# Performance work log

Measured on AMD Instinct MI355X. Metric: run time of the kernel, lower is better.

Reference implementation:

```python
import jax, jax.numpy as jnp
import numpy as np

B, T, INP, OUT, H = 64, 512, 256, 256, 512


def _uniform(key, shape, scale):
    return jax.random.uniform(key, shape, jnp.float32, -scale, scale)


def lstm_proj(x, w_ih, w_hh, b, w_hr):
    """Single-layer LSTM with projection (torch nn.LSTM proj_size semantics).
    x: [B,T,D], w_ih: [4H,D], w_hh: [4H,P], b: [4H] (b_ih+b_hh), w_hr: [P,H].
    Returns hidden sequence [B,T,P]. Gate order: i, f, g, o."""
    # Precompute input contribution for all timesteps: [T,B,4H]
    xg = jnp.einsum('btd,gd->tbg', x, w_ih) + b
    Bsz = x.shape[0]
    P, Hh = w_hr.shape
    h0 = jnp.zeros((Bsz, P), x.dtype)
    c0 = jnp.zeros((Bsz, Hh), x.dtype)

    def step(carry, xg_t):
        h, c = carry
        gates = xg_t + h @ w_hh.T          # [B,4H]
        i, f, g, o = jnp.split(gates, 4, axis=-1)
        c = jax.nn.sigmoid(f) * c + jax.nn.sigmoid(i) * jnp.tanh(g)
        h = (jax.nn.sigmoid(o) * jnp.tanh(c)) @ w_hr.T  # projected hidden [B,P]
        return (h, c), h

    _, hs = jax.lax.scan(step, (h0, c0), xg)
    return hs.transpose(1, 0, 2)  # [B,T,P]


def setup_inputs() -> dict:
    key = jax.random.key(0)
    ks = jax.random.split(key, 10)
    s = 1.0 / np.sqrt(H)
    inp = jax.random.normal(ks[0], (B, T, INP), jnp.float32)
    out = jax.random.normal(ks[1], (B, T, OUT), jnp.float32)
    # lstm: input INP -> hidden H, proj OUT
    w_ih1 = _uniform(ks[2], (4 * H, INP), s)
    w_hh1 = _uniform(ks[3], (4 * H, OUT), s)
    b1 = _uniform(ks[4], (4 * H,), s) * 2.0  # b_ih + b_hh combined
    w_hr1 = _uniform(ks[5], (OUT, H), s)
    # lstm_reverse: input OUT -> hidden H, proj INP
    w_ih2 = _uniform(ks[6], (4 * H, OUT), s)
    w_hh2 = _uniform(ks[7], (4 * H, INP), s)
    b2 = _uniform(ks[8], (4 * H,), s) * 2.0
    w_hr2 = _uniform(ks[9], (INP, H), s)
    return {"inp": inp, "out": out,
            "w_ih1": w_ih1, "w_hh1": w_hh1, "b1": b1, "w_hr1": w_hr1,
            "w_ih2": w_ih2, "w_hh2": w_hh2, "b2": b2, "w_hr2": w_hr2}


def reference(inp, out, w_ih1, w_hh1, b1, w_hr1, w_ih2, w_hh2, b2, w_hr2):
    out2 = lstm_proj(inp, w_ih1, w_hh1, b1, w_hr1)   # [B,T,OUT]
    inp2 = lstm_proj(out, w_ih2, w_hh2, b2, w_hr2)   # [B,T,INP]
    return (inp2, out2)
```

## Files before the change

kernel.cpp:

```cpp
#include <hip/hip_runtime.h>

constexpr int kB = 64, kT = 512, kD = 256, kH = 512, kG = 2048;
constexpr int kNB = 256, kNT = 256;

typedef __attribute__((ext_vector_type(8))) short bf16x8;
typedef __attribute__((ext_vector_type(4))) float f32x4;
typedef unsigned long long ull;
union U4 { unsigned u[4]; ull q[2]; bf16x8 v; };

__device__ __forceinline__ ushort f2bf(float x) {
    union { float f; unsigned u; } v; v.f = x;
    unsigned r = v.u + 0x7FFFu + ((v.u >> 16) & 1u);
    return (ushort)(r >> 16);
}
__device__ __forceinline__ unsigned pk2(float a, float b) {
    return (unsigned)f2bf(a) | ((unsigned)f2bf(b) << 16);
}
__device__ __forceinline__ float sigm(float x) { return 1.f / (1.f + __expf(-x)); }

#define AT_LOAD(p)     __hip_atomic_load((p), __ATOMIC_RELAXED, __HIP_MEMORY_SCOPE_AGENT)
#define AT_LOAD64(p)   __hip_atomic_load((p), __ATOMIC_RELAXED, __HIP_MEMORY_SCOPE_AGENT)
#define AT_STORE(p,v)  __hip_atomic_store((p), (v), __ATOMIC_RELAXED, __HIP_MEMORY_SCOPE_AGENT)
#define AT_ADD(p,v)    __hip_atomic_fetch_add((p), (v), __ATOMIC_RELAXED, __HIP_MEMORY_SCOPE_AGENT)
#define VMCNT0() asm volatile("s_waitcnt vmcnt(0)" ::: "memory")

__device__ __forceinline__ unsigned ld_dw(const unsigned* p, bool fast) {
    unsigned r;
    if (fast) asm volatile("global_load_dword %0, %1, off sc0\n\ts_waitcnt vmcnt(0)"
                           : "=&v"(r) : "v"(p) : "memory");
    else r = AT_LOAD(p);
    return r;
}
__device__ __forceinline__ void ld8q(const ull* p, ull* q, bool fast) {
    if (fast) {
        asm volatile(
            "global_load_dwordx2 %0, %8, off sc0\n\t"
            "global_load_dwordx2 %1, %8, off offset:8 sc0\n\t"
            "global_load_dwordx2 %2, %8, off offset:16 sc0\n\t"
            "global_load_dwordx2 %3, %8, off offset:24 sc0\n\t"
            "global_load_dwordx2 %4, %8, off offset:32 sc0\n\t"
            "global_load_dwordx2 %5, %8, off offset:40 sc0\n\t"
            "global_load_dwordx2 %6, %8, off offset:48 sc0\n\t"
            "global_load_dwordx2 %7, %8, off offset:56 sc0\n\t"
            "s_waitcnt vmcnt(0)"
            : "=&v"(q[0]), "=&v"(q[1]), "=&v"(q[2]), "=&v"(q[3]),
              "=&v"(q[4]), "=&v"(q[5]), "=&v"(q[6]), "=&v"(q[7])
            : "v"(p) : "memory");
    } else {
        #pragma unroll
        for (int i = 0; i < 8; i++) q[i] = AT_LOAD64(p + i);
    }
}
__device__ __forceinline__ void st_u16(ushort* p, ushort v, bool fast) {
    if (fast) *p = v;
    else __hip_atomic_store(p, v, __ATOMIC_RELAXED, __HIP_MEMORY_SCOPE_AGENT);
}
__device__ __forceinline__ void st_dw(unsigned* p, unsigned v, bool fast) {
    if (fast) *p = v;
    else AT_STORE(p, v);
}

__global__ void bar_init_kernel(unsigned* ws) {
    AT_STORE(ws + threadIdx.x, 0u);
}

__global__ void __launch_bounds__(kNT, 1) lstm2_kernel(
    const float* __restrict__ x1, const float* __restrict__ x2,
    const float* __restrict__ wih1, const float* __restrict__ whh1,
    const float* __restrict__ b1,   const float* __restrict__ whr1,
    const float* __restrict__ wih2, const float* __restrict__ whh2,
    const float* __restrict__ b2,   const float* __restrict__ whr2,
    float* __restrict__ out, unsigned* __restrict__ ws)
{
    const int bid = blockIdx.x, tid = threadIdx.x;
    const int team = bid & 7, rank = bid >> 3;
    const int l = team >> 2, bteam = team & 3, blkh = rank;
    const int h0 = blkh * 16, grow0 = bteam * 16;

    const float* x   = l ? x2 : x1;
    const float* wih = l ? wih2 : wih1;
    const float* whh = l ? whh2 : whh1;
    const float* bb  = l ? b2 : b1;
    const float* whr = l ? whr2 : whr1;
    float* outp = out + (l ? (size_t)0 : (size_t)kB * kT * kD);

    unsigned* TG  = ws + 256;
    unsigned* XC  = ws + 768;
    unsigned* SDB = ws + 1024;
    unsigned* WC  = ws + 66560;

    __shared__ unsigned sst[16 * 268];
    __shared__ float lgs[4][16][17];

    __builtin_amdgcn_fence(__ATOMIC_SEQ_CST, "agent");
    VMCNT0();

    unsigned xcc;
    asm volatile("s_getreg_b32 %0, hwreg(HW_REG_XCC_ID)" : "=s"(xcc));
    xcc &= 15u;
    if (tid == 0) AT_STORE(XC + bid, xcc);

    {
        const int wlin = bteam * 32 + rank;
        const int j  = wlin * 16 + (tid >> 4);
        const int k0 = (tid & 15) * 32;
        const float* whh_r = whh + (size_t)j * kD;
        float acc[32];
        #pragma unroll
        for (int i = 0; i < 32; i++) acc[i] = 0.f;
        for (int p = 0; p < kD; p++) {
            float w = whh_r[p];
            const float4* wr = (const float4*)(whr + (size_t)p * kH + k0);
            #pragma unroll
            for (int q = 0; q < 8; q++) {
                float4 v = wr[q];
                acc[q*4+0] = fmaf(w, v.x, acc[q*4+0]);
                acc[q*4+1] = fmaf(w, v.y, acc[q*4+1]);
                acc[q*4+2] = fmaf(w, v.z, acc[q*4+2]);
                acc[q*4+3] = fmaf(w, v.w, acc[q*4+3]);
            }
        }
        unsigned* dst = WC + (size_t)l * kG * 256 + (size_t)j * 256 + k0 / 2;
        #pragma unroll
        for (int i = 0; i < 16; i++) AT_STORE(dst + i, pk2(acc[2*i], acc[2*i+1]));
    }
    VMCNT0();
    __syncthreads();
    if (tid == 0) {
        unsigned a = AT_ADD(ws + 0, 1u);
        if (a == (unsigned)(kNB - 1)) AT_STORE(ws + 64, 1u);
        while (AT_LOAD(ws + 64) == 0u) __builtin_amdgcn_s_sleep(2);
    }
    __syncthreads();

    const int lane = tid & 63;
    unsigned x0 = AT_LOAD(XC + team);
    unsigned xr = (lane < 32) ? AT_LOAD(XC + team + 8 * lane) : x0;
    const bool fast = __all((int)(xr == x0));

    if (rank == 0 && tid < 64) st_dw(TG + team * 64 + tid, 0u, fast);
    if (tid < 128) {
        st_dw(SDB + (size_t)(team * 2 + 0) * 4096 + rank * 128 + tid, 0u, fast);
        st_dw(SDB + (size_t)(team * 2 + 1) * 4096 + rank * 128 + tid, 0u, fast);
    }

    const int wv = tid >> 6;
    const int n = lane & 15, kq = lane >> 4;
    const int gcol = wv * kH + h0 + n;
    const float bias = bb[gcol];
    const int mrow = grow0 + n;
    const int crow = tid >> 4, ccol = tid & 15;

    bf16x8 bxh[8];
    #pragma unroll
    for (int ks = 0; ks < 8; ks++) {
        const float4* p = (const float4*)(wih + (size_t)gcol * kD + ks * 32 + kq * 8);
        float4 a0 = p[0], a1 = p[1];
        U4 h;
        h.u[0] = pk2(a0.x, a0.y); h.u[1] = pk2(a0.z, a0.w);
        h.u[2] = pk2(a1.x, a1.y); h.u[3] = pk2(a1.z, a1.w);
        bxh[ks] = h.v;
    }
    bf16x8 bsh[16];
    {
        const ull* wcp = (const ull*)(WC + (size_t)l * kG * 256 + (size_t)gcol * 256);
        #pragma unroll
        for (int ks = 0; ks < 16; ks++) {
            U4 u;
            u.q[0] = AT_LOAD64(wcp + ks * 8 + kq * 2 + 0);
            u.q[1] = AT_LOAD64(wcp + ks * 8 + kq * 2 + 1);
            bsh[ks] = u.v;
        }
    }
    const bool isProj = (blkh < 16);
    bf16x8 bp[16];
    if (isProj) {
        const int pcol = blkh * 16 + n;
        #pragma unroll
        for (int ks = 0; ks < 16; ks++) {
            const float4* p = (const float4*)(whr + (size_t)pcol * kH + ks * 32 + kq * 8);
            float4 a0 = p[0], a1 = p[1];
            U4 h;
            h.u[0] = pk2(a0.x, a0.y); h.u[1] = pk2(a0.z, a0.w);
            h.u[2] = pk2(a1.x, a1.y); h.u[3] = pk2(a1.z, a1.w);
            bp[ks] = h.v;
        }
    }
    bf16x8 ax[8];
    #pragma unroll
    for (int ks = 0; ks < 8; ks++) {
        const float4* xp = (const float4*)(x + (size_t)mrow * kT * kD + ks * 32 + kq * 8);
        float4 a0 = xp[0], a1 = xp[1];
        U4 f;
        f.u[0] = pk2(a0.x, a0.y); f.u[1] = pk2(a0.z, a0.w);
        f.u[2] = pk2(a1.x, a1.y); f.u[3] = pk2(a1.z, a1.w);
        ax[ks] = f.v;
    }
    float creg = 0.f;
    const int srow = tid >> 4, scol = (tid & 15) * 16;

    VMCNT0();
    __syncthreads();
    if (tid == 0) {
        unsigned a = AT_ADD(ws + 128, 1u);
        if (a == (unsigned)(kNB - 1)) AT_STORE(ws + 192, 1u);
        while (AT_LOAD(ws + 192) == 0u) __builtin_amdgcn_s_sleep(2);
    }
    __syncthreads();

    for (int t = 0; t <= kT; ++t) {
        if (t == kT && !isProj) break;
        const int par = (t + 1) & 1;
        const unsigned want = (unsigned)t;
        const unsigned* tagp = TG + (team * 2 + par) * 32;
        while (true) {
            unsigned tg = want;
            if (lane < 32) tg = ld_dw(tagp + lane, fast);
            if (__all((int)(tg >= want))) break;
        }
        __builtin_amdgcn_sched_barrier(0);

        {
            const ull* sp = (const ull*)(SDB + (size_t)(team * 2 + par) * 4096
                                             + srow * 256 + scol);
            ull q[8];
            ld8q(sp, q, fast);
            ull* ld = (ull*)&sst[srow * 268 + scol];
            #pragma unroll
            for (int i = 0; i < 8; i++) ld[i] = q[i];
        }
        __syncthreads();
        bf16x8 as[16];
        #pragma unroll
        for (int ks = 0; ks < 16; ks++)
            as[ks] = *(const bf16x8*)&sst[n * 268 + ks * 16 + kq * 4];

        if (t < kT) {
            f32x4 c0 = {bias, bias, bias, bias};
            f32x4 c1 = {0.f, 0.f, 0.f, 0.f};
            f32x4 c2 = {0.f, 0.f, 0.f, 0.f};
            #pragma unroll
            for (int ks = 0; ks < 8; ks++) {
                c0 = __builtin_amdgcn_mfma_f32_16x16x32_bf16(ax[ks],   bxh[ks],   c0, 0, 0, 0);
                c1 = __builtin_amdgcn_mfma_f32_16x16x32_bf16(as[ks],   bsh[ks],   c1, 0, 0, 0);
                c2 = __builtin_amdgcn_mfma_f32_16x16x32_bf16(as[8+ks], bsh[8+ks], c2, 0, 0, 0);
            }
            #pragma unroll
            for (int r = 0; r < 4; r++)
                lgs[wv][kq * 4 + r][n] = c0[r] + c1[r] + c2[r];
            __syncthreads();
            const float gi = sigm(lgs[0][crow][ccol]);
            const float gf = sigm(lgs[1][crow][ccol]);
            const float gg = tanhf(lgs[2][crow][ccol]);
            const float go = sigm(lgs[3][crow][ccol]);
            creg = gf * creg + gi * gg;
            const float sv = go * tanhf(creg);
            ushort* sd = (ushort*)(SDB + (size_t)(team * 2 + (t & 1)) * 4096);
            st_u16(sd + crow * 512 + h0 + ccol, f2bf(sv), fast);
            VMCNT0();
            __syncthreads();
            if (tid == 0)
                st_dw(TG + (team * 2 + (t & 1)) * 32 + rank, (unsigned)(t + 1), fast);
        }

        if (t >= 1 && isProj) {
            f32x4 p0 = {0.f, 0.f, 0.f, 0.f};
            f32x4 p1 = {0.f, 0.f, 0.f, 0.f};
            #pragma unroll
            for (int ks = 0; ks < 8; ks++) {
                p0 = __builtin_amdgcn_mfma_f32_16x16x32_bf16(as[ks],     bp[ks],     p0, 0, 0, 0);
                p1 = __builtin_amdgcn_mfma_f32_16x16x32_bf16(as[8 + ks], bp[8 + ks], p1, 0, 0, 0);
            }
            const int pcol = blkh * 16 + n;
            #pragma unroll
            for (int r = 0; r < 4; r++)
                outp[((size_t)(grow0 + kq * 4 + r) * kT + (t - 1)) * kD + pcol] = p0[r] + p1[r];
        }

        if (t + 1 < kT) {
            #pragma unroll
            for (int ks = 0; ks < 8; ks++) {
                const float4* xp = (const float4*)(x + ((size_t)mrow * kT + (t + 1)) * kD + ks * 32 + kq * 8);
                float4 a0 = xp[0], a1 = xp[1];
                U4 f;
                f.u[0] = pk2(a0.x, a0.y); f.u[1] = pk2(a0.z, a0.w);
                f.u[2] = pk2(a1.x, a1.y); f.u[3] = pk2(a1.z, a1.w);
                ax[ks] = f.v;
            }
        }
    }
}

extern "C" void kernel_launch(void* const* d_in, const int* in_sizes, int n_in,
                              void* d_out, int out_size, void* d_ws, size_t ws_size,
                              hipStream_t stream) {
    const float* x1   = (const float*)d_in[0];
    const float* x2   = (const float*)d_in[1];
    const float* wih1 = (const float*)d_in[2];
    const float* whh1 = (const float*)d_in[3];
    const float* b1   = (const float*)d_in[4];
    const float* whr1 = (const float*)d_in[5];
    const float* wih2 = (const float*)d_in[6];
    const float* whh2 = (const float*)d_in[7];
    const float* b2   = (const float*)d_in[8];
    const float* whr2 = (const float*)d_in[9];
    float* outp  = (float*)d_out;
    unsigned* ws = (unsigned*)d_ws;

    bar_init_kernel<<<1, 1024, 0, stream>>>(ws);
    lstm2_kernel<<<dim3(kNB), dim3(kNT), 0, stream>>>(
        x1, x2, wih1, whh1, b1, whr1, wih2, whh2, b2, whr2, outp, ws);
}
```

Measured before the change: 2.938 ms.

## Split recurrent state wait into four chunks overlapped with MFMA compute

Each step now runs the input-projection MFMAs before waiting on other blocks. The per-step wait on peer tags is then split into four groups of eight producers, and each group's 16-byte slice of the hidden state is loaded and consumed by MFMAs as soon as it arrives. This is meant to overlap cross-block synchronisation latency with matrix work instead of waiting for all 32 producers first. It also changes the tag store to an explicit sc0 store with a wait, and adds three more __syncthreads per step, which could cost more than the overlap saves.

```diff
diff --git a/kernel.cpp b/kernel.cpp
--- a/kernel.cpp
+++ b/kernel.cpp
@@ -5,8 +5,9 @@
 
 typedef __attribute__((ext_vector_type(8))) short bf16x8;
 typedef __attribute__((ext_vector_type(4))) float f32x4;
+typedef __attribute__((ext_vector_type(4))) unsigned u32x4;
 typedef unsigned long long ull;
-union U4 { unsigned u[4]; ull q[2]; bf16x8 v; };
+union U4 { unsigned u[4]; ull q[2]; bf16x8 v; u32x4 w; };
 
 __device__ __forceinline__ ushort f2bf(float x) {
     union { float f; unsigned u; } v; v.f = x;
@@ -31,24 +32,15 @@
     else r = AT_LOAD(p);
     return r;
 }
-__device__ __forceinline__ void ld8q(const ull* p, ull* q, bool fast) {
+__device__ __forceinline__ void ld16B(const unsigned* p, unsigned* q, bool fast) {
     if (fast) {
-        asm volatile(
-            "global_load_dwordx2 %0, %8, off sc0\n\t"
-            "global_load_dwordx2 %1, %8, off offset:8 sc0\n\t"
-            "global_load_dwordx2 %2, %8, off offset:16 sc0\n\t"
-            "global_load_dwordx2 %3, %8, off offset:24 sc0\n\t"
-            "global_load_dwordx2 %4, %8, off offset:32 sc0\n\t"
-            "global_load_dwordx2 %5, %8, off offset:40 sc0\n\t"
-            "global_load_dwordx2 %6, %8, off offset:48 sc0\n\t"
-            "global_load_dwordx2 %7, %8, off offset:56 sc0\n\t"
-            "s_waitcnt vmcnt(0)"
-            : "=&v"(q[0]), "=&v"(q[1]), "=&v"(q[2]), "=&v"(q[3]),
-              "=&v"(q[4]), "=&v"(q[5]), "=&v"(q[6]), "=&v"(q[7])
-            : "v"(p) : "memory");
+        u32x4 r;
+        asm volatile("global_load_dwordx4 %0, %1, off sc0\n\ts_waitcnt vmcnt(0)"
+                     : "=&v"(r) : "v"(p) : "memory");
+        q[0] = r[0]; q[1] = r[1]; q[2] = r[2]; q[3] = r[3];
     } else {
-        #pragma unroll
-        for (int i = 0; i < 8; i++) q[i] = AT_LOAD64(p + i);
+        q[0] = AT_LOAD(p + 0); q[1] = AT_LOAD(p + 1);
+        q[2] = AT_LOAD(p + 2); q[3] = AT_LOAD(p + 3);
     }
 }
 __device__ __forceinline__ void st_u16(ushort* p, ushort v, bool fast) {
@@ -57,6 +49,11 @@
 }
 __device__ __forceinline__ void st_dw(unsigned* p, unsigned v, bool fast) {
     if (fast) *p = v;
+    else AT_STORE(p, v);
+}
+__device__ __forceinline__ void st_tag(unsigned* p, unsigned v, bool fast) {
+    if (fast) asm volatile("global_store_dword %0, %1, off sc0\n\ts_waitcnt vmcnt(0)"
+                           :: "v"(p), "v"(v) : "memory");
     else AT_STORE(p, v);
 }
 
@@ -89,7 +86,7 @@
     unsigned* SDB = ws + 1024;
     unsigned* WC  = ws + 66560;
 
-    __shared__ unsigned sst[16 * 268];
+    __shared__ __align__(16) unsigned sst[16 * 268];
     __shared__ float lgs[4][16][17];
 
     __builtin_amdgcn_fence(__ATOMIC_SEQ_CST, "agent");
@@ -197,7 +194,7 @@
         ax[ks] = f.v;
     }
     float creg = 0.f;
-    const int srow = tid >> 4, scol = (tid & 15) * 16;
+    const int srow = tid >> 4, sc4 = (tid & 15) * 4;
 
     VMCNT0();
     __syncthreads();
@@ -213,38 +210,47 @@
         const int par = (t + 1) & 1;
         const unsigned want = (unsigned)t;
         const unsigned* tagp = TG + (team * 2 + par) * 32;
-        while (true) {
-            unsigned tg = want;
-            if (lane < 32) tg = ld_dw(tagp + lane, fast);
-            if (__all((int)(tg >= want))) break;
-        }
-        __builtin_amdgcn_sched_barrier(0);
-
-        {
-            const ull* sp = (const ull*)(SDB + (size_t)(team * 2 + par) * 4096
-                                             + srow * 256 + scol);
-            ull q[8];
-            ld8q(sp, q, fast);
-            ull* ld = (ull*)&sst[srow * 268 + scol];
-            #pragma unroll
-            for (int i = 0; i < 8; i++) ld[i] = q[i];
-        }
-        __syncthreads();
+        const unsigned* slab = SDB + (size_t)(team * 2 + par) * 4096;
+
+        f32x4 c0 = {bias, bias, bias, bias};
+        if (t < kT) {
+            #pragma unroll
+            for (int ks = 0; ks < 8; ks++)
+                c0 = __builtin_amdgcn_mfma_f32_16x16x32_bf16(ax[ks], bxh[ks], c0, 0, 0, 0);
+        }
+
+        f32x4 c1 = {0.f, 0.f, 0.f, 0.f};
+        f32x4 c2 = {0.f, 0.f, 0.f, 0.f};
         bf16x8 as[16];
         #pragma unroll
-        for (int ks = 0; ks < 16; ks++)
-            as[ks] = *(const bf16x8*)&sst[n * 268 + ks * 16 + kq * 4];
+        for (int c = 0; c < 4; ++c) {
+            while (true) {
+                unsigned tg = want;
+                if (lane < 8) tg = ld_dw(tagp + 8 * c + lane, fast);
+                if (__all((int)(tg >= want))) break;
+            }
+            __builtin_amdgcn_sched_barrier(0);
+            unsigned qv[4];
+            ld16B(slab + srow * 256 + 64 * c + sc4, qv, fast);
+            *(u32x4*)&sst[srow * 268 + 64 * c + sc4] = *(u32x4*)qv;
+            __syncthreads();
+            #pragma unroll
+            for (int j = 0; j < 4; ++j)
+                as[4 * c + j] = *(const bf16x8*)&sst[n * 268 + (4 * c + j) * 16 + kq * 4];
+            if (t < kT) {
+                if (c & 1) {
+                    #pragma unroll
+                    for (int j = 0; j < 4; ++j)
+                        c2 = __builtin_amdgcn_mfma_f32_16x16x32_bf16(as[4*c+j], bsh[4*c+j], c2, 0, 0, 0);
+                } else {
+                    #pragma unroll
+                    for (int j = 0; j < 4; ++j)
+                        c1 = __builtin_amdgcn_mfma_f32_16x16x32_bf16(as[4*c+j], bsh[4*c+j], c1, 0, 0, 0);
+                }
+            }
+        }
 
         if (t < kT) {
-            f32x4 c0 = {bias, bias, bias, bias};
-            f32x4 c1 = {0.f, 0.f, 0.f, 0.f};
-            f32x4 c2 = {0.f, 0.f, 0.f, 0.f};
-            #pragma unroll
-            for (int ks = 0; ks < 8; ks++) {
-                c0 = __builtin_amdgcn_mfma_f32_16x16x32_bf16(ax[ks],   bxh[ks],   c0, 0, 0, 0);
-                c1 = __builtin_amdgcn_mfma_f32_16x16x32_bf16(as[ks],   bsh[ks],   c1, 0, 0, 0);
-                c2 = __builtin_amdgcn_mfma_f32_16x16x32_bf16(as[8+ks], bsh[8+ks], c2, 0, 0, 0);
-            }
             #pragma unroll
             for (int r = 0; r < 4; r++)
                 lgs[wv][kq * 4 + r][n] = c0[r] + c1[r] + c2[r];
@@ -260,7 +266,7 @@
             VMCNT0();
             __syncthreads();
             if (tid == 0)
-                st_dw(TG + (team * 2 + (t & 1)) * 32 + rank, (unsigned)(t + 1), fast);
+                st_tag(TG + (team * 2 + (t & 1)) * 32 + rank, (unsigned)(t + 1), fast);
         }
 
         if (t >= 1 && isProj) {
```

Result: slower. 3.291 ms (+12.0%).

## Replace tag-based step barrier with per-element step-tagged hidden state

Applied to the files above, without the earlier changes.

Each hidden-state element is now stored as a 32-bit word that carries the step number in its high 16 bits next to the bf16 value. Consumers spin on the data itself until every tag matches the current step. This removes the separate tag array, the vmcnt drain, the extra block barrier and the tag store that each step previously needed. The input-projection MFMAs are also hoisted ahead of the spin so they overlap the wait. In exchange the exchange buffer doubles in size, each poll reads twice as many bytes, and correctness depends on 32-bit stores being observed atomically.

```diff
diff --git a/kernel.cpp b/kernel.cpp
--- a/kernel.cpp
+++ b/kernel.cpp
@@ -5,8 +5,9 @@
 
 typedef __attribute__((ext_vector_type(8))) short bf16x8;
 typedef __attribute__((ext_vector_type(4))) float f32x4;
+typedef __attribute__((ext_vector_type(4))) unsigned u32x4;
 typedef unsigned long long ull;
-union U4 { unsigned u[4]; ull q[2]; bf16x8 v; };
+union U4 { unsigned u[4]; ull q[2]; bf16x8 v; u32x4 w; };
 
 __device__ __forceinline__ ushort f2bf(float x) {
     union { float f; unsigned u; } v; v.f = x;
@@ -24,36 +25,30 @@
 #define AT_ADD(p,v)    __hip_atomic_fetch_add((p), (v), __ATOMIC_RELAXED, __HIP_MEMORY_SCOPE_AGENT)
 #define VMCNT0() asm volatile("s_waitcnt vmcnt(0)" ::: "memory")
 
-__device__ __forceinline__ unsigned ld_dw(const unsigned* p, bool fast) {
-    unsigned r;
-    if (fast) asm volatile("global_load_dword %0, %1, off sc0\n\ts_waitcnt vmcnt(0)"
-                           : "=&v"(r) : "v"(p) : "memory");
-    else r = AT_LOAD(p);
-    return r;
-}
-__device__ __forceinline__ void ld8q(const ull* p, ull* q, bool fast) {
+__device__ __forceinline__ void ld128B(const unsigned* p, unsigned* q, bool fast) {
     if (fast) {
+        u32x4 r0, r1, r2, r3, r4, r5, r6, r7;
         asm volatile(
-            "global_load_dwordx2 %0, %8, off sc0\n\t"
-            "global_load_dwordx2 %1, %8, off offset:8 sc0\n\t"
-            "global_load_dwordx2 %2, %8, off offset:16 sc0\n\t"
-            "global_load_dwordx2 %3, %8, off offset:24 sc0\n\t"
-            "global_load_dwordx2 %4, %8, off offset:32 sc0\n\t"
-            "global_load_dwordx2 %5, %8, off offset:40 sc0\n\t"
-            "global_load_dwordx2 %6, %8, off offset:48 sc0\n\t"
-            "global_load_dwordx2 %7, %8, off offset:56 sc0\n\t"
+            "global_load_dwordx4 %0, %8, off sc0\n\t"
+            "global_load_dwordx4 %1, %8, off offset:16 sc0\n\t"
+            "global_load_dwordx4 %2, %8, off offset:32 sc0\n\t"
+            "global_load_dwordx4 %3, %8, off offset:48 sc0\n\t"
+            "global_load_dwordx4 %4, %8, off offset:64 sc0\n\t"
+            "global_load_dwordx4 %5, %8, off offset:80 sc0\n\t"
+            "global_load_dwordx4 %6, %8, off offset:96 sc0\n\t"
+            "global_load_dwordx4 %7, %8, off offset:112 sc0\n\t"
             "s_waitcnt vmcnt(0)"
-            : "=&v"(q[0]), "=&v"(q[1]), "=&v"(q[2]), "=&v"(q[3]),
-              "=&v"(q[4]), "=&v"(q[5]), "=&v"(q[6]), "=&v"(q[7])
+            : "=&v"(r0), "=&v"(r1), "=&v"(r2), "=&v"(r3),
+              "=&v"(r4), "=&v"(r5), "=&v"(r6), "=&v"(r7)
             : "v"(p) : "memory");
+        *(u32x4*)(q + 0)  = r0; *(u32x4*)(q + 4)  = r1;
+        *(u32x4*)(q + 8)  = r2; *(u32x4*)(q + 12) = r3;
+        *(u32x4*)(q + 16) = r4; *(u32x4*)(q + 20) = r5;
+        *(u32x4*)(q + 24) = r6; *(u32x4*)(q + 28) = r7;
     } else {
         #pragma unroll
-        for (int i = 0; i < 8; i++) q[i] = AT_LOAD64(p + i);
-    }
-}
-__device__ __forceinline__ void st_u16(ushort* p, ushort v, bool fast) {
-    if (fast) *p = v;
-    else __hip_atomic_store(p, v, __ATOMIC_RELAXED, __HIP_MEMORY_SCOPE_AGENT);
+        for (int i = 0; i < 16; i++) ((ull*)q)[i] = AT_LOAD64((const ull*)p + i);
+    }
 }
 __device__ __forceinline__ void st_dw(unsigned* p, unsigned v, bool fast) {
     if (fast) *p = v;
@@ -84,12 +79,11 @@
     const float* whr = l ? whr2 : whr1;
     float* outp = out + (l ? (size_t)0 : (size_t)kB * kT * kD);
 
-    unsigned* TG  = ws + 256;
     unsigned* XC  = ws + 768;
     unsigned* SDB = ws + 1024;
-    unsigned* WC  = ws + 66560;
-
-    __shared__ unsigned sst[16 * 268];
+    unsigned* WC  = ws + 132096;
+
+    __shared__ __align__(16) unsigned sst[16 * 268];
     __shared__ float lgs[4][16][17];
 
     __builtin_amdgcn_fence(__ATOMIC_SEQ_CST, "agent");
@@ -138,11 +132,8 @@
     unsigned xr = (lane < 32) ? AT_LOAD(XC + team + 8 * lane) : x0;
     const bool fast = __all((int)(xr == x0));
 
-    if (rank == 0 && tid < 64) st_dw(TG + team * 64 + tid, 0u, fast);
-    if (tid < 128) {
-        st_dw(SDB + (size_t)(team * 2 + 0) * 4096 + rank * 128 + tid, 0u, fast);
-        st_dw(SDB + (size_t)(team * 2 + 1) * 4096 + rank * 128 + tid, 0u, fast);
-    }
+    st_dw(SDB + (size_t)(team * 2 + 0) * 8192 + rank * 256 + tid, 0u, fast);
+    st_dw(SDB + (size_t)(team * 2 + 1) * 8192 + rank * 256 + tid, 0u, fast);
 
     const int wv = tid >> 6;
     const int n = lane & 15, kq = lane >> 4;
@@ -197,7 +188,9 @@
         ax[ks] = f.v;
     }
     float creg = 0.f;
-    const int srow = tid >> 4, scol = (tid & 15) * 16;
+    const int srow = tid >> 4;
+    const int c32  = (tid & 15) * 32;
+    const int sc16 = (tid & 15) * 16;
 
     VMCNT0();
     __syncthreads();
@@ -211,24 +204,31 @@
     for (int t = 0; t <= kT; ++t) {
         if (t == kT && !isProj) break;
         const int par = (t + 1) & 1;
-        const unsigned want = (unsigned)t;
-        const unsigned* tagp = TG + (team * 2 + par) * 32;
-        while (true) {
-            unsigned tg = want;
-            if (lane < 32) tg = ld_dw(tagp + lane, fast);
-            if (__all((int)(tg >= want))) break;
+        const unsigned* slab = SDB + (size_t)(team * 2 + par) * 8192;
+
+        f32x4 c0 = {bias, bias, bias, bias};
+        if (t < kT) {
+            #pragma unroll
+            for (int ks = 0; ks < 8; ks++)
+                c0 = __builtin_amdgcn_mfma_f32_16x16x32_bf16(ax[ks], bxh[ks], c0, 0, 0, 0);
+        }
+
+        unsigned v[32];
+        {
+            const unsigned* myp = slab + srow * 512 + c32;
+            const unsigned want = (unsigned)t;
+            while (true) {
+                ld128B(myp, v, fast);
+                bool ok = true;
+                #pragma unroll
+                for (int i = 0; i < 32; i++) ok &= ((v[i] >> 16) == want);
+                if (__all((int)ok)) break;
+            }
         }
         __builtin_amdgcn_sched_barrier(0);
-
-        {
-            const ull* sp = (const ull*)(SDB + (size_t)(team * 2 + par) * 4096
-                                             + srow * 256 + scol);
-            ull q[8];
-            ld8q(sp, q, fast);
-            ull* ld = (ull*)&sst[srow * 268 + scol];
-            #pragma unroll
-            for (int i = 0; i < 8; i++) ld[i] = q[i];
-        }
+        #pragma unroll
+        for (int j = 0; j < 16; j++)
+            sst[srow * 268 + sc16 + j] = (v[2*j] & 0xffffu) | (v[2*j+1] << 16);
         __syncthreads();
         bf16x8 as[16];
         #pragma unroll
@@ -236,18 +236,16 @@
             as[ks] = *(const bf16x8*)&sst[n * 268 + ks * 16 + kq * 4];
 
         if (t < kT) {
-            f32x4 c0 = {bias, bias, bias, bias};
-            f32x4 c1 = {0.f, 0.f, 0.f, 0.f};
-            f32x4 c2 = {0.f, 0.f, 0.f, 0.f};
+            f32x4 a1 = {0.f, 0.f, 0.f, 0.f};
+            f32x4 a2 = {0.f, 0.f, 0.f, 0.f};
             #pragma unroll
             for (int ks = 0; ks < 8; ks++) {
-                c0 = __builtin_amdgcn_mfma_f32_16x16x32_bf16(ax[ks],   bxh[ks],   c0, 0, 0, 0);
-                c1 = __builtin_amdgcn_mfma_f32_16x16x32_bf16(as[ks],   bsh[ks],   c1, 0, 0, 0);
-                c2 = __builtin_amdgcn_mfma_f32_16x16x32_bf16(as[8+ks], bsh[8+ks], c2, 0, 0, 0);
+                a1 = __builtin_amdgcn_mfma_f32_16x16x32_bf16(as[ks],   bsh[ks],   a1, 0, 0, 0);
+                a2 = __builtin_amdgcn_mfma_f32_16x16x32_bf16(as[8+ks], bsh[8+ks], a2, 0, 0, 0);
             }
             #pragma unroll
             for (int r = 0; r < 4; r++)
-                lgs[wv][kq * 4 + r][n] = c0[r] + c1[r] + c2[r];
+                lgs[wv][kq * 4 + r][n] = c0[r] + a1[r] + a2[r];
             __syncthreads();
             const float gi = sigm(lgs[0][crow][ccol]);
             const float gf = sigm(lgs[1][crow][ccol]);
@@ -255,12 +253,9 @@
             const float go = sigm(lgs[3][crow][ccol]);
             creg = gf * creg + gi * gg;
             const float sv = go * tanhf(creg);
-            ushort* sd = (ushort*)(SDB + (size_t)(team * 2 + (t & 1)) * 4096);
-            st_u16(sd + crow * 512 + h0 + ccol, f2bf(sv), fast);
-            VMCNT0();
-            __syncthreads();
-            if (tid == 0)
-                st_dw(TG + (team * 2 + (t & 1)) * 32 + rank, (unsigned)(t + 1), fast);
+            unsigned* sd = SDB + (size_t)(team * 2 + (t & 1)) * 8192;
+            st_dw(sd + crow * 512 + h0 + ccol,
+                  ((unsigned)(t + 1) << 16) | (unsigned)f2bf(sv), fast);
         }
 
         if (t >= 1 && isProj) {
@@ -281,10 +276,10 @@
             #pragma unroll
             for (int ks = 0; ks < 8; ks++) {
                 const float4* xp = (const float4*)(x + ((size_t)mrow * kT + (t + 1)) * kD + ks * 32 + kq * 8);
-                float4 a0 = xp[0], a1 = xp[1];
+                float4 a0 = xp[0], a1v = xp[1];
                 U4 f;
-                f.u[0] = pk2(a0.x, a0.y); f.u[1] = pk2(a0.z, a0.w);
-                f.u[2] = pk2(a1.x, a1.y); f.u[3] = pk2(a1.z, a1.w);
+                f.u[0] = pk2(a0.x, a0.y);  f.u[1] = pk2(a0.z, a0.w);
+                f.u[2] = pk2(a1v.x, a1v.y); f.u[3] = pk2(a1v.z, a1v.w);
                 ax[ks] = f.v;
             }
         }
```

Measured after the change: 3.270 ms. 1.11x slower.
